# Optimization experiments

Hardware: AMD Instinct MI355X
Metric: run time of the kernel (lower is better)

Reference implementation:

```python
import jax, jax.numpy as jnp
import numpy as np

M = 7                 # RoIAlign output size
S = 1                 # bilinear samples per bin per axis
SPATIAL_SCALE = 1.0 / 16.0
NUM_CLASSES = 21
SCORE_THRESH = 0.05
NMS_THRESH = 0.5
NUM_DET = 100
MIN_SIZE = 1.0
REG_W = (10.0, 10.0, 5.0, 5.0)
BBOX_CLIP = float(np.log(1000.0 / 16.0))
NEG = -1e9


def setup_inputs():
    key = jax.random.key(0)
    ks = jax.random.split(key, 8)
    H, W, C, N, HID = 50, 50, 256, 1000, 1024
    feature = jax.random.normal(ks[0], (H, W, C), jnp.float32)
    ctr = jax.random.uniform(ks[1], (N, 2), jnp.float32, 50.0, 750.0)
    wh = jax.random.uniform(ks[2], (N, 2), jnp.float32, 20.0, 300.0)
    proposal = jnp.concatenate([jnp.clip(ctr - wh / 2, 0.0, 800.0),
                                jnp.clip(ctr + wh / 2, 0.0, 800.0)], axis=1)
    D = C * M * M  # 12544
    sc = 0.02
    return dict(
        feature=feature, proposal=proposal,
        w1=jax.random.normal(ks[3], (D, HID), jnp.float32) * sc,
        b1=jnp.zeros((HID,), jnp.float32),
        w2=jax.random.normal(ks[4], (HID, HID), jnp.float32) * sc,
        b2=jnp.zeros((HID,), jnp.float32),
        w_cls=jax.random.normal(ks[5], (HID, NUM_CLASSES), jnp.float32) * sc,
        b_cls=jnp.zeros((NUM_CLASSES,), jnp.float32),
        w_box=jax.random.normal(ks[6], (HID, NUM_CLASSES * 4), jnp.float32) * sc,
        b_box=jnp.zeros((NUM_CLASSES * 4,), jnp.float32),
        img_h=800, img_w=800)


def _bilinear(feat, ys, xs):
    # feat [H,W,C]; ys [N,P]; xs [N,Q] -> [N,P,Q,C], zero outside image
    H, W, _ = feat.shape
    y = jnp.broadcast_to(ys[:, :, None], (ys.shape[0], ys.shape[1], xs.shape[1]))
    x = jnp.broadcast_to(xs[:, None, :], y.shape)
    oob = (y < -1.0) | (y > H) | (x < -1.0) | (x > W)
    y = jnp.clip(y, 0.0, H - 1.0)
    x = jnp.clip(x, 0.0, W - 1.0)
    y0 = jnp.floor(y).astype(jnp.int32)
    x0 = jnp.floor(x).astype(jnp.int32)
    y1 = jnp.minimum(y0 + 1, H - 1)
    x1 = jnp.minimum(x0 + 1, W - 1)
    ly, lx = y - y0, x - x0
    hy, hx = 1.0 - ly, 1.0 - lx
    v = (feat[y0, x0] * (hy * hx)[..., None] + feat[y0, x1] * (hy * lx)[..., None]
         + feat[y1, x0] * (ly * hx)[..., None] + feat[y1, x1] * (ly * lx)[..., None])
    return jnp.where(oob[..., None], 0.0, v)


def _roi_align(feat, rois):
    # feat [H,W,C], rois [N,4] in image coords -> [N, C*M*M]
    r = rois * SPATIAL_SCALE
    x1, y1 = r[:, 0], r[:, 1]
    rw = jnp.maximum(r[:, 2] - x1, 1.0)
    rh = jnp.maximum(r[:, 3] - y1, 1.0)
    off = (jnp.arange(M, dtype=jnp.float32)[:, None]
           + (jnp.arange(S, dtype=jnp.float32) + 0.5)[None, :] / S).reshape(-1)  # [M*S]
    ys = y1[:, None] + off[None, :] * (rh / M)[:, None]
    xs = x1[:, None] + off[None, :] * (rw / M)[:, None]
    g = _bilinear(feat, ys, xs)                                  # [N,MS,MS,C]
    N, _, _, C = g.shape
    g = g.reshape(N, M, S, M, S, C).mean(axis=(2, 4))            # [N,M,M,C]
    return g.transpose(0, 3, 1, 2).reshape(N, C * M * M)


def _decode(deltas, boxes):
    # deltas [L,N,4] (per class), boxes [N,4]
    wx, wy, ww, wh = REG_W
    w = boxes[:, 2] - boxes[:, 0]
    h = boxes[:, 3] - boxes[:, 1]
    cx = boxes[:, 0] + 0.5 * w
    cy = boxes[:, 1] + 0.5 * h
    dx, dy = deltas[..., 0] / wx, deltas[..., 1] / wy
    dw = jnp.minimum(deltas[..., 2] / ww, BBOX_CLIP)
    dh = jnp.minimum(deltas[..., 3] / wh, BBOX_CLIP)
    pcx, pcy = dx * w + cx, dy * h + cy
    pw, ph = jnp.exp(dw) * w, jnp.exp(dh) * h
    return jnp.stack([pcx - 0.5 * pw, pcy - 0.5 * ph,
                      pcx + 0.5 * pw, pcy + 0.5 * ph], axis=-1)


def _iou_one(box, boxes):
    lt = jnp.maximum(box[:2], boxes[:, :2])
    rb = jnp.minimum(box[2:], boxes[:, 2:])
    wh = jnp.clip(rb - lt, 0.0)
    inter = wh[:, 0] * wh[:, 1]
    a1 = (box[2] - box[0]) * (box[3] - box[1])
    a2 = (boxes[:, 2] - boxes[:, 0]) * (boxes[:, 3] - boxes[:, 1])
    return inter / (a1 + a2 - inter + 1e-9)


def _nms(boxes, scores):
    # fixed-shape greedy NMS: NUM_DET selections, invalid slots masked to NEG
    def step(s, _):
        i = jnp.argmax(s)
        sc, b = s[i], boxes[i]
        supp = _iou_one(b, boxes) > NMS_THRESH
        s = jnp.where(supp, NEG, s).at[i].set(NEG)
        return s, (b, sc)
    _, (kb, ksc) = jax.lax.scan(step, scores, None, length=NUM_DET)
    valid = ksc > NEG * 0.5
    return jnp.where(valid[:, None], kb, 0.0), jnp.where(valid, ksc, 0.0)


def _forward(feature, proposal, w1, b1, w2, b2, w_cls, b_cls, w_box, b_box, img_h, img_w):
    pooled = _roi_align(feature, proposal)                # [N, 12544]
    h = jax.nn.relu(pooled @ w1 + b1)
    h = jax.nn.relu(h @ w2 + b2)
    logits = h @ w_cls + b_cls                            # [N, 21]
    deltas = (h @ w_box + b_box).reshape(-1, NUM_CLASSES, 4)
    pred_score = jax.nn.softmax(logits, axis=-1)
    cls_scores = pred_score[:, 1:].T                      # [L, N], L = 20 fg classes
    cls_deltas = jnp.swapaxes(deltas[:, 1:], 0, 1)        # [L, N, 4]
    boxes = _decode(cls_deltas, proposal)                 # [L, N, 4]
    boxes = jnp.stack([jnp.clip(boxes[..., 0], 0.0, img_w),
                       jnp.clip(boxes[..., 1], 0.0, img_h),
                       jnp.clip(boxes[..., 2], 0.0, img_w),
                       jnp.clip(boxes[..., 3], 0.0, img_h)], axis=-1)
    bw = boxes[..., 2] - boxes[..., 0]
    bh = boxes[..., 3] - boxes[..., 1]
    keep = (bw >= MIN_SIZE) & (bh >= MIN_SIZE) & (cls_scores >= SCORE_THRESH)
    masked = jnp.where(keep, cls_scores, NEG)
    kb, ksc = jax.vmap(_nms)(boxes, masked)               # [L,K,4], [L,K]
    labels = jnp.broadcast_to(jnp.arange(1, NUM_CLASSES, dtype=jnp.int32)[:, None], ksc.shape)
    return kb.reshape(-1, 4), ksc.reshape(-1), labels.reshape(-1)


def reference(feature, proposal, w1, b1, w2, b2, w_cls, b_cls, w_box, b_box, img_h, img_w):
    return _forward(feature, proposal, w1, b1, w2, b2, w_cls, b_cls, w_box, b_box,
                    float(img_h), float(img_w))
```

## Files before the change

### kernel.cpp

```cpp
#include <hip/hip_runtime.h>


#define NEGV -1000000000.0f

typedef __attribute__((ext_vector_type(8))) short short8v;
typedef __attribute__((ext_vector_type(4))) float f32x4;

#define KDIM 12544
#define PL   (1024 * 12544)

__device__ __forceinline__ unsigned short to_bf16(float f) {
    unsigned u = __float_as_uint(f);
    unsigned r = u + 0x7FFFu + ((u >> 16) & 1u);
    return (unsigned short)(r >> 16);
}
__device__ __forceinline__ float bf2f(unsigned short s) {
    return __uint_as_float((unsigned)s << 16);
}
__device__ __forceinline__ void gload16(const void* gsrc, void* ldst) {
    __builtin_amdgcn_global_load_lds(
        (const __attribute__((address_space(1))) unsigned int*)gsrc,
        (__attribute__((address_space(3))) unsigned int*)ldst,
        16, 0, 0);
}

__global__ __launch_bounds__(256) void roi_align_split3(const float* __restrict__ feat,
    const float* __restrict__ prop, unsigned short* __restrict__ Ap)
{
    int n = blockIdx.y;
    int p = blockIdx.x;
    int my = p / 7, mx = p % 7;
    float x1 = prop[n * 4 + 0] * 0.0625f;
    float y1 = prop[n * 4 + 1] * 0.0625f;
    float x2 = prop[n * 4 + 2] * 0.0625f;
    float y2 = prop[n * 4 + 3] * 0.0625f;
    float rw = fmaxf(x2 - x1, 1.0f), rh = fmaxf(y2 - y1, 1.0f);
    float y = y1 + ((float)my + 0.5f) * (rh / 7.0f);
    float x = x1 + ((float)mx + 0.5f) * (rw / 7.0f);
    bool oob = (y < -1.0f) || (y > 50.0f) || (x < -1.0f) || (x > 50.0f);
    y = fminf(fmaxf(y, 0.0f), 49.0f);
    x = fminf(fmaxf(x, 0.0f), 49.0f);
    int y0 = (int)floorf(y), x0 = (int)floorf(x);
    int y1i = min(y0 + 1, 49), x1i = min(x0 + 1, 49);
    float ly = y - (float)y0, lx = x - (float)x0;
    float hy = 1.0f - ly, hx = 1.0f - lx;
    int c = threadIdx.x;
    float v = feat[(y0 * 50 + x0) * 256 + c] * (hy * hx)
            + feat[(y0 * 50 + x1i) * 256 + c] * (hy * lx)
            + feat[(y1i * 50 + x0) * 256 + c] * (ly * hx)
            + feat[(y1i * 50 + x1i) * 256 + c] * (ly * lx);
    if (oob) v = 0.0f;
    unsigned short s1 = to_bf16(v);  float r  = v - bf2f(s1);
    unsigned short s2 = to_bf16(r);  float r2 = r - bf2f(s2);
    unsigned short s3 = to_bf16(r2);
    size_t o = (size_t)n * KDIM + p * 256 + c;
    Ap[o] = s1; Ap[PL + o] = s2; Ap[2 * (size_t)PL + o] = s3;
}

__global__ __launch_bounds__(256) void convT_k(const float* __restrict__ src,
    unsigned short* __restrict__ dst, int perm, int Ktot)
{
    __shared__ unsigned short T[3][64][72];
    int k0 = blockIdx.x * 64;
    int n0 = blockIdx.y * 64;
    int t = threadIdx.x;
    size_t plst = (size_t)1024 * Ktot;
#pragma unroll
    for (int j = 0; j < 16; ++j) {
        int idx = t + 256 * j;
        int n_l = idx & 63, k_l = idx >> 6;
        int kp = k0 + k_l;
        int orow = perm ? ((kp & 255) * 49 + (kp >> 8)) : kp;
        float v = src[(size_t)orow * 1024 + n0 + n_l];
        unsigned short s1 = to_bf16(v);  float r  = v - bf2f(s1);
        unsigned short s2 = to_bf16(r);  float r2 = r - bf2f(s2);
        T[0][k_l][n_l] = s1;
        T[1][k_l][n_l] = s2;
        T[2][k_l][n_l] = to_bf16(r2);
    }
    __syncthreads();
#pragma unroll
    for (int p = 0; p < 3; ++p)
#pragma unroll
        for (int jj = 0; jj < 2; ++jj) {
            int w = t + 256 * jj;
            int n_l = w >> 3, kg = w & 7;
            short8v pk;
#pragma unroll
            for (int e = 0; e < 8; ++e) pk[e] = (short)T[p][kg * 8 + e][n_l];
            *(short8v*)&dst[p * plst + (size_t)(n0 + n_l) * Ktot + k0 + kg * 8] = pk;
        }
}

__global__ __launch_bounds__(256) void conv_heads_k(const float* __restrict__ w_cls,
    const float* __restrict__ w_box, unsigned short* __restrict__ Bth)
{
    int id = blockIdx.x * 256 + threadIdx.x;
    int j = id >> 10, k = id & 1023;
    float v = 0.f;
    if (j < 21) v = w_cls[k * 21 + j];
    else if (j < 105) v = w_box[k * 84 + (j - 21)];
    unsigned short s1 = to_bf16(v);  float r  = v - bf2f(s1);
    unsigned short s2 = to_bf16(r);  float r2 = r - bf2f(s2);
    Bth[id] = s1; Bth[131072 + id] = s2; Bth[262144 + id] = to_bf16(r2);
}

__device__ __forceinline__ void gemm_body(const unsigned short* __restrict__ Ap,
    const unsigned short* __restrict__ Bp, float* __restrict__ part,
    int K, int Ks, int nks, size_t plA, size_t plB, int N,
    int col0, int row0, int z, unsigned short* lds)
{
    int t = threadIdx.x;
    int w = t >> 6, lane = t & 63;
    int ln = lane & 15, g = lane >> 4;
    int wr = (w >> 1) * 64, wc = (w & 1) * 64;

    const unsigned short* smat = (w >= 2) ? Bp : Ap;
    size_t spl = (w >= 2) ? plB : plA;
    int sbase = (w >= 2) ? col0 : row0;
    int hoff = (w >= 2) ? 24576 : 0;
    int j0 = (w & 1) * 12;
    int srow = lane >> 2;
    int scol = ((lane & 3) ^ ((lane >> 3) & 3)) * 8;
    int kOff = z * Ks;

    auto stage = [&](int buf, int ks) {
        char* lb = (char*)lds + buf * 49152 + hoff;
        int kpos = kOff + (ks << 5) + scol;
#pragma unroll
        for (int ii = 0; ii < 12; ++ii) {
            int j = j0 + ii;
            int p = j >> 3, rb = j & 7;
            const unsigned short* src = smat + (size_t)p * spl
                + (size_t)(sbase + rb * 16 + srow) * K + kpos;
            gload16(src, lb + p * 8192 + rb * 1024);
        }
    };

    f32x4 acc[4][4] = {};
    stage(0, 0);
    __syncthreads();
    int buf = 0;
    for (int ks = 0; ks < nks; ++ks) {
        if (ks + 1 < nks) stage(buf ^ 1, ks + 1);
        const unsigned short* la  = (const unsigned short*)((char*)lds + buf * 49152);
        const unsigned short* lbB = (const unsigned short*)((char*)lds + buf * 49152 + 24576);
#pragma unroll
        for (int pb = 0; pb < 3; ++pb) {
            short8v bf[4];
#pragma unroll
            for (int fc = 0; fc < 4; ++fc) {
                int r = wc + fc * 16 + ln;
                bf[fc] = *(const short8v*)&lbB[pb * 4096 + r * 32 + ((g ^ ((r >> 1) & 3)) << 3)];
            }
#pragma unroll
            for (int pa = 0; pa < 3 - pb; ++pa) {
                short8v af[4];
#pragma unroll
                for (int fr = 0; fr < 4; ++fr) {
                    int r = wr + fr * 16 + ln;
                    af[fr] = *(const short8v*)&la[pa * 4096 + r * 32 + ((g ^ ((r >> 1) & 3)) << 3)];
                }
#pragma unroll
                for (int fr = 0; fr < 4; ++fr)
#pragma unroll
                    for (int fc = 0; fc < 4; ++fc)
                        acc[fr][fc] = __builtin_amdgcn_mfma_f32_16x16x32_bf16(
                            af[fr], bf[fc], acc[fr][fc], 0, 0, 0);
            }
        }
        __syncthreads();
        buf ^= 1;
    }
    float* dst = part + (size_t)z * 1024 * N;
    int rbase = row0 + wr, cbase = col0 + wc;
#pragma unroll
    for (int fr = 0; fr < 4; ++fr)
#pragma unroll
        for (int fc = 0; fc < 4; ++fc)
#pragma unroll
            for (int reg = 0; reg < 4; ++reg)
                dst[(size_t)(rbase + fr * 16 + g * 4 + reg) * N + cbase + fc * 16 + ln] =
                    acc[fr][fc][reg];
}

__global__ __launch_bounds__(256, 1) void gemm1_k(const unsigned short* __restrict__ Ap,
    const unsigned short* __restrict__ Bp, float* __restrict__ part)
{
    extern __shared__ unsigned short ldsdyn[];
    int b = blockIdx.x;
    int xcd = b & 7;
    int rest = b >> 3;
    int m = rest & 7;
    int qhi = rest >> 3;
    int q = xcd + 8 * qhi;
    int z  = q >> 3;
    int qz = q & 7;
    int col0 = ((qz & 1) * 4 + (m & 3)) * 128;
    int row0 = ((qz >> 1) * 2 + (m >> 2)) * 128;
    gemm_body(Ap, Bp, part, KDIM, 1568, 49, (size_t)PL, (size_t)PL, 1024,
              col0, row0, z, ldsdyn);
}

__global__ __launch_bounds__(256, 1) void gemm_g_k(const unsigned short* __restrict__ Ap,
    const unsigned short* __restrict__ Bp, float* __restrict__ part,
    int K, int Ks, int nks, int plA, int plB, int N)
{
    extern __shared__ unsigned short ldsdyn[];
    gemm_body(Ap, Bp, part, K, Ks, nks, (size_t)plA, (size_t)plB, N,
              blockIdx.x * 128, blockIdx.y * 128, blockIdx.z, ldsdyn);
}

__global__ __launch_bounds__(256) void reduce_split3_k(const float* __restrict__ part,
    const float* __restrict__ bias, unsigned short* __restrict__ dstP, int S)
{
    int m = blockIdx.x, t = threadIdx.x;
    size_t o = (size_t)m * 1024 + t * 4;
    float4 acc = *(const float4*)&part[o];
    for (int s = 1; s < S; ++s) {
        float4 p = *(const float4*)&part[(size_t)s * 1048576 + o];
        acc.x += p.x; acc.y += p.y; acc.z += p.z; acc.w += p.w;
    }
    float4 bv = *(const float4*)&bias[t * 4];
    float vals[4] = { fmaxf(acc.x + bv.x, 0.f), fmaxf(acc.y + bv.y, 0.f),
                      fmaxf(acc.z + bv.z, 0.f), fmaxf(acc.w + bv.w, 0.f) };
    unsigned short o1[4], o2[4], o3[4];
#pragma unroll
    for (int e = 0; e < 4; ++e) {
        unsigned short s1 = to_bf16(vals[e]);  float r  = vals[e] - bf2f(s1);
        unsigned short s2 = to_bf16(r);        float r2 = r - bf2f(s2);
        o1[e] = s1; o2[e] = s2; o3[e] = to_bf16(r2);
    }
    *(uint2*)&dstP[o]           = *(uint2*)o1;
    *(uint2*)&dstP[1048576 + o] = *(uint2*)o2;
    *(uint2*)&dstP[2097152 + o] = *(uint2*)o3;
}

__global__ __launch_bounds__(128) void reduce_heads_k(const float* __restrict__ part,
    const float* __restrict__ b_cls, const float* __restrict__ b_box,
    float* __restrict__ Hout)
{
    int m = blockIdx.x, t = threadIdx.x;
    size_t o = (size_t)m * 128 + t;
    float a = part[o];
    for (int s = 1; s < 8; ++s) a += part[(size_t)s * 131072 + o];
    float b = (t < 21) ? b_cls[t] : (t < 105 ? b_box[t - 21] : 0.f);
    Hout[o] = a + b;
}

__global__ __launch_bounds__(64) void postproc_k(const float* __restrict__ H,
    const float* __restrict__ prop, const int* __restrict__ img_h_p,
    const int* __restrict__ img_w_p, float* __restrict__ scores_m,
    float* __restrict__ boxes_dec)
{
    int n = blockIdx.x;
    int cls = threadIdx.x;
    if (cls < 1 || cls > 20) return;
    const float* hn = H + (size_t)n * 128;
    float mx = -3.0e38f;
    for (int i = 0; i < 21; ++i) mx = fmaxf(mx, hn[i]);
    float sum = 0.f;
    for (int i = 0; i < 21; ++i) sum += expf(hn[i] - mx);
    float score = expf(hn[cls] - mx) / sum;

    float p0 = prop[n * 4 + 0], p1 = prop[n * 4 + 1];
    float p2 = prop[n * 4 + 2], p3 = prop[n * 4 + 3];
    float w = p2 - p0, h = p3 - p1;
    float cx = p0 + 0.5f * w, cy = p1 + 0.5f * h;
    float d0 = hn[21 + cls * 4 + 0];
    float d1 = hn[21 + cls * 4 + 1];
    float d2 = hn[21 + cls * 4 + 2];
    float d3 = hn[21 + cls * 4 + 3];
    const float CLIP = 4.135166556742356f;
    float dx = d0 / 10.0f, dy = d1 / 10.0f;
    float dw = fminf(d2 / 5.0f, CLIP), dh = fminf(d3 / 5.0f, CLIP);
    float pcx = dx * w + cx, pcy = dy * h + cy;
    float pw = expf(dw) * w, ph = expf(dh) * h;
    float bx1 = pcx - 0.5f * pw, by1 = pcy - 0.5f * ph;
    float bx2 = pcx + 0.5f * pw, by2 = pcy + 0.5f * ph;
    float iw = (float)img_w_p[0], ih = (float)img_h_p[0];
    bx1 = fminf(fmaxf(bx1, 0.f), iw);
    by1 = fminf(fmaxf(by1, 0.f), ih);
    bx2 = fminf(fmaxf(bx2, 0.f), iw);
    by2 = fminf(fmaxf(by2, 0.f), ih);
    float bw = bx2 - bx1, bh = by2 - by1;
    bool keep = (bw >= 1.0f) && (bh >= 1.0f) && (score >= 0.05f);
    int o = (cls - 1) * 1000 + n;
    scores_m[o] = keep ? score : NEGV;
    ((float4*)boxes_dec)[o] = make_float4(bx1, by1, bx2, by2);
}

__global__ __launch_bounds__(256) void nms_sort_k(const float* __restrict__ scores_m,
    const float* __restrict__ boxes_dec, float* __restrict__ sboxes,
    float* __restrict__ sscore, int* __restrict__ Vcnt)
{
    __shared__ unsigned long long sk[1024];
    __shared__ int cnt;
    int cls = blockIdx.x, t = threadIdx.x;
    if (t == 0) cnt = 0;
    __syncthreads();
    for (int r = t; r < 1024; r += 256) {
        unsigned long long inv = ~0ull;
        if (r < 1000) {
            float v = scores_m[cls * 1000 + r];
            unsigned ub = __float_as_uint(v);
            ub = (ub & 0x80000000u) ? ~ub : (ub | 0x80000000u);
            inv = ~(((unsigned long long)ub << 32) | (unsigned)(1023 - r));
            if (v > 0.5f * NEGV) atomicAdd(&cnt, 1);
        }
        sk[r] = inv;
    }
    __syncthreads();
    for (int k = 2; k <= 1024; k <<= 1) {
        for (int j = k >> 1; j > 0; j >>= 1) {
            for (int pi = t; pi < 512; pi += 256) {
                int i = ((pi & ~(j - 1)) << 1) | (pi & (j - 1));
                int p = i | j;
                bool up = ((i & k) == 0);
                unsigned long long a = sk[i], b2 = sk[p];
                if ((a > b2) == up) { sk[i] = b2; sk[p] = a; }
            }
            __syncthreads();
        }
    }
    for (int r = t; r < 1024; r += 256) {
        unsigned long long key = ~sk[r];
        unsigned ub = (unsigned)(key >> 32);
        int idx = 1023 - (int)(key & 1023u);
        float4 bx = make_float4(0.f, 0.f, 0.f, 0.f);
        float scv = NEGV;
        if (key != 0ull && idx < 1000) {
            bx = ((const float4*)boxes_dec)[cls * 1000 + idx];
            unsigned u = (ub & 0x80000000u) ? (ub & 0x7FFFFFFFu) : ~ub;
            scv = __uint_as_float(u);
        }
        ((float4*)sboxes)[(size_t)cls * 1024 + r] = bx;
        sscore[(size_t)cls * 1024 + r] = scv;
    }
    if (t == 0) Vcnt[cls] = cnt;
}

__global__ __launch_bounds__(256) void nms_mask_k(const float* __restrict__ sboxes,
    unsigned long long* __restrict__ mask)
{
    __shared__ float4 colb[1024];
    __shared__ float area[1024];
    int cls = blockIdx.x >> 4;
    int chunk = blockIdx.x & 15;
    int t = threadIdx.x;
    const float4* sb = (const float4*)sboxes + (size_t)cls * 1024;
    for (int j = t; j < 1024; j += 256) {
        float4 b = sb[j];
        colb[j] = b;
        area[j] = (b.z - b.x) * (b.w - b.y);
    }
    __syncthreads();
    int row_l = t >> 2;
    int qt = t & 3;
    int i = chunk * 64 + row_l;
    float4 rb = colb[i];
    float a1 = area[i];
    unsigned long long* dst = mask + ((size_t)cls * 1024 + i) * 16 + qt * 4;
#pragma unroll
    for (int w = 0; w < 4; ++w) {
        unsigned long long wv = 0;
        int jb = qt * 256 + w * 64;
#pragma unroll 8
        for (int bi = 0; bi < 64; ++bi) {
            int j = jb + bi;
            float4 cb = colb[j];
            float ltx = fmaxf(rb.x, cb.x), lty = fmaxf(rb.y, cb.y);
            float rbx = fminf(rb.z, cb.z), rby = fminf(rb.w, cb.w);
            float wiw = fmaxf(rbx - ltx, 0.f), wih = fmaxf(rby - lty, 0.f);
            float inter = wiw * wih;
            float iou = inter / (a1 + area[j] - inter + 1e-9f);
            if (j > i && iou > 0.5f) wv |= (1ull << bi);
        }
        dst[w] = wv;
    }
}

__global__ __launch_bounds__(64) void nms_sweep_k(const float* __restrict__ sboxes,
    const float* __restrict__ sscore, const int* __restrict__ Vcnt,
    const unsigned long long* __restrict__ mask, float* __restrict__ out)
{
    int cls = blockIdx.x;
    int lane = threadIdx.x;
    __shared__ int keptlist[100];
    int V = Vcnt[cls];
    const unsigned long long* mbase = mask + (size_t)cls * 1024 * 16;
    unsigned long long suppr = 0;
    int kept = 0;
    int nb = (V + 15) >> 4;
    for (int b = 0; b < nb && kept < 100; ++b) {
        unsigned long long L[16];
#pragma unroll
        for (int k = 0; k < 16; ++k)
            L[k] = mbase[(size_t)(b * 16 + k) * 16 + (lane & 15)];
#pragma unroll
        for (int k = 0; k < 16; ++k) {
            int i = b * 16 + k;
            if (i < V && kept < 100) {
                bool sup = (lane == (i >> 6)) && ((suppr >> (i & 63)) & 1ull);
                if (__ballot(sup) == 0ull) {
                    if (lane == 0) keptlist[kept] = i;
                    if (lane < 16) suppr |= L[k];
                    ++kept;
                }
            }
        }
    }
    __syncthreads();
    float* kb   = out;
    float* ksc  = out + 8000;
    float* klab = out + 10000;
    for (int s = lane; s < 100; s += 64) {
        klab[cls * 100 + s] = (float)(cls + 1);
        if (s < kept) {
            int r = keptlist[s];
            ((float4*)kb)[cls * 100 + s] =
                ((const float4*)sboxes)[(size_t)cls * 1024 + r];
            ksc[cls * 100 + s] = sscore[(size_t)cls * 1024 + r];
        } else {
            ((float4*)kb)[cls * 100 + s] = make_float4(0.f, 0.f, 0.f, 0.f);
            ksc[cls * 100 + s] = 0.f;
        }
    }
}

extern "C" void kernel_launch(void* const* d_in, const int* in_sizes, int n_in,
                              void* d_out, int out_size, void* d_ws, size_t ws_size,
                              hipStream_t stream)
{
    const float* feat  = (const float*)d_in[0];
    const float* prop  = (const float*)d_in[1];
    const float* w1    = (const float*)d_in[2];
    const float* b1    = (const float*)d_in[3];
    const float* w2    = (const float*)d_in[4];
    const float* b2    = (const float*)d_in[5];
    const float* w_cls = (const float*)d_in[6];
    const float* b_cls = (const float*)d_in[7];
    const float* w_box = (const float*)d_in[8];
    const float* b_box = (const float*)d_in[9];
    const int* img_h   = (const int*)d_in[10];
    const int* img_w   = (const int*)d_in[11];

    (void)hipFuncSetAttribute(reinterpret_cast<const void*>(gemm1_k),
                              hipFuncAttributeMaxDynamicSharedMemorySize, 98304);
    (void)hipFuncSetAttribute(reinterpret_cast<const void*>(gemm_g_k),
                              hipFuncAttributeMaxDynamicSharedMemorySize, 98304);

    char* wsb = (char*)d_ws;
    unsigned short* Apl = (unsigned short*)wsb;
    unsigned short* Bpl = (unsigned short*)(wsb + 77070336);
    float* part = (float*)(wsb + 154140672);
    unsigned short* Ap2 = (unsigned short*)wsb;
    unsigned short* Bt2 = (unsigned short*)(wsb + 6291456);
    unsigned short* Bth = (unsigned short*)(wsb + 12582912);
    unsigned short* Ah  = (unsigned short*)(wsb + 13369344);
    float* scores_m  = (float*)(wsb + 187695104);
    float* boxes_dec = (float*)(wsb + 187775104);
    float* Hout      = (float*)(wsb + 188095104);
    unsigned long long* nmask = (unsigned long long*)(wsb + 154140672);
    float* sboxes = (float*)(wsb + 156762112);
    float* sscore = (float*)(wsb + 157089792);
    int*   Vcnt   = (int*)(wsb + 157171712);
    float* outp = (float*)d_out;

    hipLaunchKernelGGL(roi_align_split3, dim3(49, 1000), dim3(256), 0, stream,
                       feat, prop, Apl);
    hipLaunchKernelGGL(convT_k, dim3(196, 16), dim3(256), 0, stream,
                       w1, Bpl, 1, KDIM);
    hipLaunchKernelGGL(gemm1_k, dim3(512), dim3(256), 98304, stream,
                       Apl, Bpl, part);
    hipLaunchKernelGGL(reduce_split3_k, dim3(1000), dim3(256), 0, stream,
                       part, b1, Ap2, 8);
    hipLaunchKernelGGL(convT_k, dim3(16, 16), dim3(256), 0, stream,
                       w2, Bt2, 0, 1024);
    hipLaunchKernelGGL(conv_heads_k, dim3(512), dim3(256), 0, stream,
                       w_cls, w_box, Bth);
    hipLaunchKernelGGL(gemm_g_k, dim3(8, 8, 4), dim3(256), 98304, stream,
                       Ap2, Bt2, part, 1024, 256, 8, 1048576, 1048576, 1024);
    hipLaunchKernelGGL(reduce_split3_k, dim3(1000), dim3(256), 0, stream,
                       part, b2, Ah, 4);
    hipLaunchKernelGGL(gemm_g_k, dim3(1, 8, 8), dim3(256), 98304, stream,
                       Ah, Bth, part, 1024, 128, 4, 1048576, 131072, 128);
    hipLaunchKernelGGL(reduce_heads_k, dim3(1000), dim3(128), 0, stream,
                       part, b_cls, b_box, Hout);
    hipLaunchKernelGGL(postproc_k, dim3(1000), dim3(64), 0, stream,
                       Hout, prop, img_h, img_w, scores_m, boxes_dec);
    hipLaunchKernelGGL(nms_sort_k, dim3(20), dim3(256), 0, stream,
                       scores_m, boxes_dec, sboxes, sscore, Vcnt);
    hipLaunchKernelGGL(nms_mask_k, dim3(320), dim3(256), 0, stream, sboxes, nmask);
    hipLaunchKernelGGL(nms_sweep_k, dim3(20), dim3(64), 0, stream,
                       sboxes, sscore, Vcnt, nmask, outp);
}
```

Before: 442.8 us.

## Single-buffer GEMM LDS for three blocks per CU and fuse heads reduce with postproc

The GEMM kernels drop the double-buffered 96KB dynamic LDS in favor of a single 48KB static buffer. Launch bounds are raised to 3 blocks per CU so occupancy, rather than in-block prefetch, hides global-load latency. A-fragments are now loaded once per k-step instead of per B-panel. The heads split-K reduction is fused with the softmax/decode postprocessing through shared memory, which removes one launch and the Hout round trip. This loses explicit load/compute overlap within a block and adds register pressure from holding all A fragments.

```diff
diff --git a/kernel.cpp b/kernel.cpp
--- a/kernel.cpp
+++ b/kernel.cpp
@@ -124,9 +124,13 @@
     int scol = ((lane & 3) ^ ((lane >> 3) & 3)) * 8;
     int kOff = z * Ks;
 
-    auto stage = [&](int buf, int ks) {
-        char* lb = (char*)lds + buf * 49152 + hoff;
+    const unsigned short* la  = lds;
+    const unsigned short* lbB = lds + 12288;
+
+    f32x4 acc[4][4] = {};
+    for (int ks = 0; ks < nks; ++ks) {
         int kpos = kOff + (ks << 5) + scol;
+        char* lb = (char*)lds + hoff;
 #pragma unroll
         for (int ii = 0; ii < 12; ++ii) {
             int j = j0 + ii;
@@ -135,16 +139,16 @@
                 + (size_t)(sbase + rb * 16 + srow) * K + kpos;
             gload16(src, lb + p * 8192 + rb * 1024);
         }
-    };
-
-    f32x4 acc[4][4] = {};
-    stage(0, 0);
-    __syncthreads();
-    int buf = 0;
-    for (int ks = 0; ks < nks; ++ks) {
-        if (ks + 1 < nks) stage(buf ^ 1, ks + 1);
-        const unsigned short* la  = (const unsigned short*)((char*)lds + buf * 49152);
-        const unsigned short* lbB = (const unsigned short*)((char*)lds + buf * 49152 + 24576);
+        __syncthreads();
+
+        short8v af[3][4];
+#pragma unroll
+        for (int pa = 0; pa < 3; ++pa)
+#pragma unroll
+            for (int fr = 0; fr < 4; ++fr) {
+                int r = wr + fr * 16 + ln;
+                af[pa][fr] = *(const short8v*)&la[pa * 4096 + r * 32 + ((g ^ ((r >> 1) & 3)) << 3)];
+            }
 #pragma unroll
         for (int pb = 0; pb < 3; ++pb) {
             short8v bf[4];
@@ -154,23 +158,15 @@
                 bf[fc] = *(const short8v*)&lbB[pb * 4096 + r * 32 + ((g ^ ((r >> 1) & 3)) << 3)];
             }
 #pragma unroll
-            for (int pa = 0; pa < 3 - pb; ++pa) {
-                short8v af[4];
-#pragma unroll
-                for (int fr = 0; fr < 4; ++fr) {
-                    int r = wr + fr * 16 + ln;
-                    af[fr] = *(const short8v*)&la[pa * 4096 + r * 32 + ((g ^ ((r >> 1) & 3)) << 3)];
-                }
+            for (int pa = 0; pa < 3 - pb; ++pa)
 #pragma unroll
                 for (int fr = 0; fr < 4; ++fr)
 #pragma unroll
                     for (int fc = 0; fc < 4; ++fc)
                         acc[fr][fc] = __builtin_amdgcn_mfma_f32_16x16x32_bf16(
-                            af[fr], bf[fc], acc[fr][fc], 0, 0, 0);
-            }
+                            af[pa][fr], bf[fc], acc[fr][fc], 0, 0, 0);
         }
         __syncthreads();
-        buf ^= 1;
     }
     float* dst = part + (size_t)z * 1024 * N;
     int rbase = row0 + wr, cbase = col0 + wc;
@@ -184,10 +180,10 @@
                     acc[fr][fc][reg];
 }
 
-__global__ __launch_bounds__(256, 1) void gemm1_k(const unsigned short* __restrict__ Ap,
+__global__ __launch_bounds__(256, 3) void gemm1_k(const unsigned short* __restrict__ Ap,
     const unsigned short* __restrict__ Bp, float* __restrict__ part)
 {
-    extern __shared__ unsigned short ldsdyn[];
+    __shared__ unsigned short lds[24576];
     int b = blockIdx.x;
     int xcd = b & 7;
     int rest = b >> 3;
@@ -199,16 +195,16 @@
     int col0 = ((qz & 1) * 4 + (m & 3)) * 128;
     int row0 = ((qz >> 1) * 2 + (m >> 2)) * 128;
     gemm_body(Ap, Bp, part, KDIM, 1568, 49, (size_t)PL, (size_t)PL, 1024,
-              col0, row0, z, ldsdyn);
-}
-
-__global__ __launch_bounds__(256, 1) void gemm_g_k(const unsigned short* __restrict__ Ap,
+              col0, row0, z, lds);
+}
+
+__global__ __launch_bounds__(256, 3) void gemm_g_k(const unsigned short* __restrict__ Ap,
     const unsigned short* __restrict__ Bp, float* __restrict__ part,
     int K, int Ks, int nks, int plA, int plB, int N)
 {
-    extern __shared__ unsigned short ldsdyn[];
+    __shared__ unsigned short lds[24576];
     gemm_body(Ap, Bp, part, K, Ks, nks, (size_t)plA, (size_t)plB, N,
-              blockIdx.x * 128, blockIdx.y * 128, blockIdx.z, ldsdyn);
+              blockIdx.x * 128, blockIdx.y * 128, blockIdx.z, lds);
 }
 
 __global__ __launch_bounds__(256) void reduce_split3_k(const float* __restrict__ part,
@@ -236,27 +232,22 @@
     *(uint2*)&dstP[2097152 + o] = *(uint2*)o3;
 }
 
-__global__ __launch_bounds__(128) void reduce_heads_k(const float* __restrict__ part,
+__global__ __launch_bounds__(128) void heads_post_k(const float* __restrict__ part,
     const float* __restrict__ b_cls, const float* __restrict__ b_box,
-    float* __restrict__ Hout)
-{
-    int m = blockIdx.x, t = threadIdx.x;
-    size_t o = (size_t)m * 128 + t;
+    const float* __restrict__ prop, const int* __restrict__ img_h_p,
+    const int* __restrict__ img_w_p, float* __restrict__ scores_m,
+    float* __restrict__ boxes_dec)
+{
+    __shared__ float hn[128];
+    int n = blockIdx.x, t = threadIdx.x;
+    size_t o = (size_t)n * 128 + t;
     float a = part[o];
     for (int s = 1; s < 8; ++s) a += part[(size_t)s * 131072 + o];
     float b = (t < 21) ? b_cls[t] : (t < 105 ? b_box[t - 21] : 0.f);
-    Hout[o] = a + b;
-}
-
-__global__ __launch_bounds__(64) void postproc_k(const float* __restrict__ H,
-    const float* __restrict__ prop, const int* __restrict__ img_h_p,
-    const int* __restrict__ img_w_p, float* __restrict__ scores_m,
-    float* __restrict__ boxes_dec)
-{
-    int n = blockIdx.x;
-    int cls = threadIdx.x;
+    hn[t] = a + b;
+    __syncthreads();
+    int cls = t;
     if (cls < 1 || cls > 20) return;
-    const float* hn = H + (size_t)n * 128;
     float mx = -3.0e38f;
     for (int i = 0; i < 21; ++i) mx = fmaxf(mx, hn[i]);
     float sum = 0.f;
@@ -285,9 +276,9 @@
     by2 = fminf(fmaxf(by2, 0.f), ih);
     float bw = bx2 - bx1, bh = by2 - by1;
     bool keep = (bw >= 1.0f) && (bh >= 1.0f) && (score >= 0.05f);
-    int o = (cls - 1) * 1000 + n;
-    scores_m[o] = keep ? score : NEGV;
-    ((float4*)boxes_dec)[o] = make_float4(bx1, by1, bx2, by2);
+    int oo = (cls - 1) * 1000 + n;
+    scores_m[oo] = keep ? score : NEGV;
+    ((float4*)boxes_dec)[oo] = make_float4(bx1, by1, bx2, by2);
 }
 
 __global__ __launch_bounds__(256) void nms_sort_k(const float* __restrict__ scores_m,
@@ -445,11 +436,6 @@
     const int* img_h   = (const int*)d_in[10];
     const int* img_w   = (const int*)d_in[11];
 
-    (void)hipFuncSetAttribute(reinterpret_cast<const void*>(gemm1_k),
-                              hipFuncAttributeMaxDynamicSharedMemorySize, 98304);
-    (void)hipFuncSetAttribute(reinterpret_cast<const void*>(gemm_g_k),
-                              hipFuncAttributeMaxDynamicSharedMemorySize, 98304);
-
     char* wsb = (char*)d_ws;
     unsigned short* Apl = (unsigned short*)wsb;
     unsigned short* Bpl = (unsigned short*)(wsb + 77070336);
@@ -460,7 +446,6 @@
     unsigned short* Ah  = (unsigned short*)(wsb + 13369344);
     float* scores_m  = (float*)(wsb + 187695104);
     float* boxes_dec = (float*)(wsb + 187775104);
-    float* Hout      = (float*)(wsb + 188095104);
     unsigned long long* nmask = (unsigned long long*)(wsb + 154140672);
     float* sboxes = (float*)(wsb + 156762112);
     float* sscore = (float*)(wsb + 157089792);
@@ -471,7 +456,7 @@
                        feat, prop, Apl);
     hipLaunchKernelGGL(convT_k, dim3(196, 16), dim3(256), 0, stream,
                        w1, Bpl, 1, KDIM);
-    hipLaunchKernelGGL(gemm1_k, dim3(512), dim3(256), 98304, stream,
+    hipLaunchKernelGGL(gemm1_k, dim3(512), dim3(256), 0, stream,
                        Apl, Bpl, part);
     hipLaunchKernelGGL(reduce_split3_k, dim3(1000), dim3(256), 0, stream,
                        part, b1, Ap2, 8);
@@ -479,16 +464,14 @@
                        w2, Bt2, 0, 1024);
     hipLaunchKernelGGL(conv_heads_k, dim3(512), dim3(256), 0, stream,
                        w_cls, w_box, Bth);
-    hipLaunchKernelGGL(gemm_g_k, dim3(8, 8, 4), dim3(256), 98304, stream,
+    hipLaunchKernelGGL(gemm_g_k, dim3(8, 8, 4), dim3(256), 0, stream,
                        Ap2, Bt2, part, 1024, 256, 8, 1048576, 1048576, 1024);
     hipLaunchKernelGGL(reduce_split3_k, dim3(1000), dim3(256), 0, stream,
                        part, b2, Ah, 4);
-    hipLaunchKernelGGL(gemm_g_k, dim3(1, 8, 8), dim3(256), 98304, stream,
+    hipLaunchKernelGGL(gemm_g_k, dim3(1, 8, 8), dim3(256), 0, stream,
                        Ah, Bth, part, 1024, 128, 4, 1048576, 131072, 128);
-    hipLaunchKernelGGL(reduce_heads_k, dim3(1000), dim3(128), 0, stream,
-                       part, b_cls, b_box, Hout);
-    hipLaunchKernelGGL(postproc_k, dim3(1000), dim3(64), 0, stream,
-                       Hout, prop, img_h, img_w, scores_m, boxes_dec);
+    hipLaunchKernelGGL(heads_post_k, dim3(1000), dim3(128), 0, stream,
+                       part, b_cls, b_box, prop, img_h, img_w, scores_m, boxes_dec);
     hipLaunchKernelGGL(nms_sort_k, dim3(20), dim3(256), 0, stream,
                        scores_m, boxes_dec, sboxes, sscore, Vcnt);
     hipLaunchKernelGGL(nms_mask_k, dim3(320), dim3(256), 0, stream, sboxes, nmask);
```

Measured after the change: 416.1 us. -6.0%, faster.
